# Kernel tuning notes

Measured on AMD Instinct MI355X. Metric: run time of the kernel, lower is better.

Reference implementation:

```python
import jax, jax.numpy as jnp
import numpy as np

EMB = 256
HEADS = 4
HD = EMB // HEADS
BS, SZ = 4, 64


def _layernorm(x, g, b, eps=1e-5):
    mu = jnp.mean(x, axis=-1, keepdims=True)
    var = jnp.mean((x - mu) ** 2, axis=-1, keepdims=True)
    return (x - mu) * jax.lax.rsqrt(var + eps) * g + b


def setup_inputs() -> dict:
    key = jax.random.key(0)
    ks = jax.random.split(key, 12)
    s = lambda k, shape, sc: jax.random.normal(k, shape, jnp.float32) * sc
    return {
        "x": s(ks[0], (BS, EMB, SZ, SZ), 1.0),
        "ln1_g": jnp.ones((EMB,), jnp.float32),
        "ln1_b": jnp.zeros((EMB,), jnp.float32),
        "wq": s(ks[1], (HD, HD), HD ** -0.5), "bq": jnp.zeros((HD,), jnp.float32),
        "wk": s(ks[2], (HD, HD), HD ** -0.5), "bk": jnp.zeros((HD,), jnp.float32),
        "wv": s(ks[3], (HD, HD), HD ** -0.5), "bv": jnp.zeros((HD,), jnp.float32),
        "wo": s(ks[4], (EMB, EMB), EMB ** -0.5), "bo": jnp.zeros((EMB,), jnp.float32),
        "ln2_g": jnp.ones((EMB,), jnp.float32),
        "ln2_b": jnp.zeros((EMB,), jnp.float32),
        "w1": s(ks[5], (EMB, EMB), EMB ** -0.5), "b1": jnp.zeros((EMB,), jnp.float32),
        "w2": s(ks[6], (EMB, EMB), EMB ** -0.5), "b2": jnp.zeros((EMB,), jnp.float32),
    }


def reference(x, ln1_g, ln1_b, wq, bq, wk, bk, wv, bv, wo, bo, ln2_g, ln2_b, w1, b1, w2, b2):
    bs, c, sz, _ = x.shape
    seq = sz * sz
    xt = x.reshape(bs, c, seq).swapaxes(1, 2)  # [b, s, c]
    xn = _layernorm(xt, ln1_g, ln1_b)
    # split heads: [b, h, s, d]
    h = xn.reshape(bs, seq, HEADS, HD).transpose(0, 2, 1, 3)
    q = h @ wq + bq
    k = h @ wk + bk
    v = h @ wv + bv
    scores = jnp.einsum("bhqd,bhkd->bhqk", q, k) / (HD ** 0.5)
    attn = jax.nn.softmax(scores, axis=-1)
    o = jnp.einsum("bhqk,bhkd->bhqd", attn, v)
    o = o.transpose(0, 2, 1, 3).reshape(bs, seq, c)
    o = o @ wo + bo
    av = o + xt  # residual 1
    ff = _layernorm(av, ln2_g, ln2_b) @ w1 + b1
    ff = jax.nn.gelu(ff, approximate=False) @ w2 + b2
    out = ff + av  # residual 2
    return out.swapaxes(1, 2).reshape(bs, c, sz, sz)
```

## Files before the change

### kernel.cpp

```cpp
#include <hip/hip_runtime.h>
#include <hip/hip_bf16.h>
#include <cstdint>

typedef __attribute__((ext_vector_type(8))) short short8;
typedef __attribute__((ext_vector_type(4))) short short4_;
typedef __attribute__((ext_vector_type(4))) float float4_;

#define MFMA16(a,b,c)  __builtin_amdgcn_mfma_f32_16x16x32_bf16(a,b,c,0,0,0)
#define MFMA16K16(a,b,c) __builtin_amdgcn_mfma_f32_16x16x16bf16_1k(a,b,c,0,0,0)
#define EXP2(x) __builtin_amdgcn_exp2f(x)

__device__ __forceinline__ short f2bs(float f) {
    union { float f; uint32_t u; } c;
    c.f = f;
    c.u += 0x7FFF + ((c.u >> 16) & 1);
    return (short)(c.u >> 16);
}
__device__ __forceinline__ float s2f(short s) {
    union { uint32_t u; float f; } c;
    c.u = ((uint32_t)(uint16_t)s) << 16;
    return c.f;
}

static const int EMB = 256;
static const int SEQ = 4096;
static const int TOK = 16384;

#define QSCALE 0.18033688011112042f

__global__ __launch_bounds__(256) void repack_kernel(
    const float* wq, const float* wk, const float* wv,
    const float* wo, const float* w1, const float* w2,
    short* wqT, short* wkT, short* wvT, short* woT, short* w1T, short* w2T)
{
    int idx = blockIdx.x * 256 + threadIdx.x;
    if (idx < 3 * 4096) {
        int m = idx / 4096, r = idx % 4096;
        int n = r / 64, k = r % 64;
        const float* src = (m == 0) ? wq : (m == 1) ? wk : wv;
        short* dst = (m == 0) ? wqT : (m == 1) ? wkT : wvT;
        float v = src[k * 64 + n];
        if (m == 0) v *= QSCALE;
        dst[n * 64 + k] = f2bs(v);
    } else {
        int idx2 = idx - 3 * 4096;
        if (idx2 < 3 * 65536) {
            int m = idx2 / 65536, r = idx2 % 65536;
            int n = r / 256, k = r % 256;
            const float* src = (m == 0) ? wo : (m == 1) ? w1 : w2;
            short* dst = (m == 0) ? woT : (m == 1) ? w1T : w2T;
            dst[n * 256 + k] = f2bs(src[k * 256 + n]);
        }
    }
}

__global__ __launch_bounds__(64) void ln1_kernel(
    const float* x, const float* g, const float* bta,
    short* xn, short* xt)
{
    int t = blockIdx.x * 64 + threadIdx.x;
    int b = t >> 12, sp = t & 4095;
    const float* xb = x + (size_t)b * EMB * SEQ + sp;
    float sum = 0.f, ss = 0.f;
#pragma unroll 32
    for (int c = 0; c < 256; c++) {
        float v = xb[(size_t)c * SEQ];
        sum += v; ss += v * v;
    }
    float mu = sum * (1.f / 256.f);
    float var = ss * (1.f / 256.f) - mu * mu;
    float rs = rsqrtf(var + 1e-5f);
    short* xnr = xn + (size_t)t * 256;
    short* xtr = xt + (size_t)t * 256;
#pragma unroll 8
    for (int c = 0; c < 256; c += 4) {
        short4_ ra, na;
#pragma unroll
        for (int j = 0; j < 4; j++) {
            float v = xb[(size_t)(c + j) * SEQ];
            ra[j] = f2bs(v);
            na[j] = f2bs((v - mu) * rs * g[c + j] + bta[c + j]);
        }
        *(short4_*)(xtr + c) = ra;
        *(short4_*)(xnr + c) = na;
    }
}

__global__ __launch_bounds__(256) void qkv_kernel(
    const short* xn, const short* wqT, const short* wkT, const short* wvT,
    const float* bq, const float* bk, const float* bv,
    short* qo, short* ko, short* vto)
{
    int tid = threadIdx.x;
    int w = tid >> 6, lane = tid & 63, quad = lane >> 4, l15 = lane & 15;
    int m0 = blockIdx.x * 64 + w * 16;
    int row = m0 + l15;
    int bb = row >> 12;
    int s0 = (m0 & 4095) + quad * 4;

    short8 a0[4], a1[4];
#pragma unroll
    for (int h = 0; h < 4; h++) {
        a0[h] = *(const short8*)(xn + (size_t)row * 256 + h * 64 + quad * 8);
        a1[h] = *(const short8*)(xn + (size_t)row * 256 + h * 64 + 32 + quad * 8);
    }

#pragma unroll
    for (int p = 0; p < 3; p++) {
        const short* WT = (p == 0) ? wqT : (p == 1) ? wkT : wvT;
        const float* bias = (p == 0) ? bq : (p == 1) ? bk : bv;
        float bscale = (p == 0) ? QSCALE : 1.f;
#pragma unroll
        for (int nb = 0; nb < 4; nb++) {
            int col = nb * 16 + l15;
            short8 b0 = *(const short8*)(WT + col * 64 + quad * 8);
            short8 b1 = *(const short8*)(WT + col * 64 + 32 + quad * 8);
            float bvv = bias[col] * bscale;
#pragma unroll
            for (int h = 0; h < 4; h++) {
                float4_ acc = {bvv, bvv, bvv, bvv};
                acc = MFMA16(a0[h], b0, acc);
                acc = MFMA16(a1[h], b1, acc);
                size_t headbase = (size_t)(bb * 4 + h) * SEQ;
                if (p < 2) {
                    short* dst = (p == 0) ? qo : ko;
#pragma unroll
                    for (int r = 0; r < 4; r++)
                        dst[(headbase + s0 + r) * 64 + col] = f2bs(acc[r]);
                } else {
                    short4_ pk;
#pragma unroll
                    for (int r = 0; r < 4; r++) pk[r] = f2bs(acc[r]);
                    *(short4_*)(vto + ((size_t)(bb * 4 + h) * 64 + col) * SEQ + s0) = pk;
                }
            }
        }
    }
}

__global__ __launch_bounds__(256, 4) void flash_kernel(
    const short* q, const short* k, const short* vt,
    short* O0, short* O1, float* l0, float* l1)
{
    __shared__ short K_lds[64 * 64];
    __shared__ short V_lds[64 * 64];

    int tid = threadIdx.x;
    int w = tid >> 6, lane = tid & 63, quad = lane >> 4, l15 = lane & 15;
    int qt = blockIdx.x, bh = blockIdx.y, grp = blockIdx.z;
    int span = 64 / gridDim.z;

    const short* qb = q + (size_t)bh * SEQ * 64;
    const short* kb = k + (size_t)bh * SEQ * 64 + (size_t)grp * span * 64 * 64;
    const short* vb = vt + (size_t)bh * 64 * SEQ + grp * span * 64;

    int qrow0 = qt * 128 + w * 32 + l15;
    int qrow1 = qrow0 + 16;
    short8 qA0 = *(const short8*)(qb + (size_t)qrow0 * 64 + quad * 8);
    short8 qA1 = *(const short8*)(qb + (size_t)qrow0 * 64 + 32 + quad * 8);
    short8 qB0 = *(const short8*)(qb + (size_t)qrow1 * 64 + quad * 8);
    short8 qB1 = *(const short8*)(qb + (size_t)qrow1 * 64 + 32 + quad * 8);

    float4_ oacc0[4], oacc1[4];
#pragma unroll
    for (int md = 0; md < 4; md++) {
        oacc0[md] = {0.f, 0.f, 0.f, 0.f};
        oacc1[md] = {0.f, 0.f, 0.f, 0.f};
    }
    float li0 = 0.f, li1 = 0.f;

    int srow = tid >> 2;
    int sr7 = srow & 7;
    int c0 = tid & 3;
    int l7 = l15 & 7;

    for (int kt = 0; kt < span; kt++) {
        __syncthreads();
#pragma unroll
        for (int i = 0; i < 2; i++) {
            int c = c0 + 4 * i;
            int dc = (c ^ sr7) << 3;
            *(short8*)&K_lds[srow * 64 + dc] =
                *(const short8*)(kb + (size_t)(kt * 64 + srow) * 64 + c * 8);
            *(short8*)&V_lds[srow * 64 + dc] =
                *(const short8*)(vb + (size_t)srow * SEQ + kt * 64 + c * 8);
        }
        __syncthreads();

        float4_ s0[4], s1[4];
#pragma unroll
        for (int nb = 0; nb < 4; nb++) {
            short8 k0 = *(const short8*)&K_lds[(nb * 16 + l15) * 64 + ((quad ^ l7) << 3)];
            short8 k1 = *(const short8*)&K_lds[(nb * 16 + l15) * 64 + (((quad + 4) ^ l7) << 3)];
            float4_ a = {0.f, 0.f, 0.f, 0.f};
            a = MFMA16(k0, qA0, a);
            a = MFMA16(k1, qA1, a);
            s0[nb] = a;
            float4_ b = {0.f, 0.f, 0.f, 0.f};
            b = MFMA16(k0, qB0, b);
            b = MFMA16(k1, qB1, b);
            s1[nb] = b;
        }

        short4_ pf0[4], pf1[4];
#pragma unroll
        for (int nb = 0; nb < 4; nb++)
#pragma unroll
            for (int r = 0; r < 4; r++) {
                float p0 = EXP2(s0[nb][r]);
                float p1 = EXP2(s1[nb][r]);
                li0 += p0; li1 += p1;
                pf0[nb][r] = f2bs(p0);
                pf1[nb][r] = f2bs(p1);
            }

#pragma unroll
        for (int md = 0; md < 4; md++)
#pragma unroll
            for (int nb = 0; nb < 4; nb++) {
                int c = nb * 2 + (quad >> 1);
                short4_ vf = *(const short4_*)&V_lds[(md * 16 + l15) * 64 +
                                                     ((c ^ l7) << 3) + ((quad & 1) << 2)];
                oacc0[md] = MFMA16K16(vf, pf0[nb], oacc0[md]);
                oacc1[md] = MFMA16K16(vf, pf1[nb], oacc1[md]);
            }
    }

    li0 += __shfl_xor(li0, 16);
    li0 += __shfl_xor(li0, 32);
    li1 += __shfl_xor(li1, 16);
    li1 += __shfl_xor(li1, 32);

    short* Op = grp ? O1 : O0;
    float* lp = grp ? l1 : l0;
    if (quad == 0) {
        lp[bh * 4096 + qrow0] = li0;
        lp[bh * 4096 + qrow1] = li1;
    }

    size_t ob0 = ((size_t)bh * 4096 + qrow0) * 64;
    size_t ob1 = ((size_t)bh * 4096 + qrow1) * 64;
#pragma unroll
    for (int md = 0; md < 4; md++) {
        short4_ pk0, pk1;
#pragma unroll
        for (int r = 0; r < 4; r++) {
            pk0[r] = f2bs(oacc0[md][r]);
            pk1[r] = f2bs(oacc1[md][r]);
        }
        *(short4_*)(Op + ob0 + md * 16 + quad * 4) = pk0;
        *(short4_*)(Op + ob1 + md * 16 + quad * 4) = pk1;
    }
}

__global__ __launch_bounds__(256) void combine_kernel(
    const short* O0, const short* O1, const float* l0, const float* l1,
    short* Oout, int two)
{
    int g = blockIdx.x * 256 + threadIdx.x;
    int qi = g >> 4;
    short4_ a = *(const short4_*)(O0 + (size_t)g * 4);
    float l = l0[qi];
    float4_ acc = {s2f(a[0]), s2f(a[1]), s2f(a[2]), s2f(a[3])};
    if (two) {
        short4_ b = *(const short4_*)(O1 + (size_t)g * 4);
        l += l1[qi];
#pragma unroll
        for (int j = 0; j < 4; j++) acc[j] += s2f(b[j]);
    }
    float inv = 1.f / l;
    short4_ pk;
#pragma unroll
    for (int j = 0; j < 4; j++) pk[j] = f2bs(acc[j] * inv);
    *(short4_*)(Oout + (size_t)g * 4) = pk;
}

__global__ __launch_bounds__(256) void mlp_kernel(
    const short* O,
    const short* woT, const short* w1T, const short* w2T,
    const float* bo, const float* b1, const float* b2,
    const float* g2, const float* be2,
    const short* xt, float* outf)
{
    __shared__ __align__(16) char smem[3 * 8448 + 128];
    short* av = (short*)smem;
    short* x2 = (short*)(smem + 8448);
    short* ff = (short*)(smem + 16896);
    float* stats = (float*)(smem + 25344);
    float* T = (float*)smem;

    int tid = threadIdx.x;
    int w = tid >> 6, lane = tid & 63, quad = lane >> 4, l15 = lane & 15;
    int m0 = blockIdx.x * 16;
    int n0 = w * 64;
    int arow = m0 + l15;
    int bbA = arow >> 12, spA = arow & 4095;

    float4_ acc[4];
#pragma unroll
    for (int nb = 0; nb < 4; nb++) {
        float bvv = bo[n0 + nb * 16 + l15];
        acc[nb] = {bvv, bvv, bvv, bvv};
    }
    for (int kc = 0; kc < 8; kc++) {
        int h = kc >> 1;
        int off = (kc & 1) * 32 + quad * 8;
        short8 a = *(const short8*)(O + ((size_t)(bbA * 4 + h) * 4096 + spA) * 64 + off);
#pragma unroll
        for (int nb = 0; nb < 4; nb++) {
            short8 b = *(const short8*)(woT + (size_t)(n0 + nb * 16 + l15) * 256 + kc * 32 + quad * 8);
            acc[nb] = MFMA16(a, b, acc[nb]);
        }
    }
#pragma unroll
    for (int nb = 0; nb < 4; nb++) {
        int col = n0 + nb * 16 + l15;
#pragma unroll
        for (int r = 0; r < 4; r++) {
            size_t t = (size_t)m0 + quad * 4 + r;
            av[(quad * 4 + r) * 264 + col] = f2bs(acc[nb][r] + s2f(xt[t * 256 + col]));
        }
    }
    __syncthreads();

    {
        int row = tid >> 4, sub = tid & 15;
        float sum = 0.f, ss = 0.f;
        short8 v0 = *(const short8*)&av[row * 264 + sub * 16];
        short8 v1 = *(const short8*)&av[row * 264 + sub * 16 + 8];
#pragma unroll
        for (int j = 0; j < 8; j++) {
            float a = s2f(v0[j]), b = s2f(v1[j]);
            sum += a + b; ss += a * a + b * b;
        }
#pragma unroll
        for (int off = 1; off < 16; off <<= 1) {
            sum += __shfl_xor(sum, off);
            ss += __shfl_xor(ss, off);
        }
        if (sub == 0) {
            float mu = sum * (1.f / 256.f);
            float var = ss * (1.f / 256.f) - mu * mu;
            stats[row] = mu;
            stats[16 + row] = rsqrtf(var + 1e-5f);
        }
    }
    __syncthreads();

    {
        int row = tid >> 4, sub = tid & 15;
        float mu = stats[row], rs = stats[16 + row];
#pragma unroll
        for (int j = 0; j < 16; j += 4) {
            int c = sub * 16 + j;
            short4_ rv = *(const short4_*)&av[row * 264 + c];
            short4_ pk;
#pragma unroll
            for (int i = 0; i < 4; i++)
                pk[i] = f2bs((s2f(rv[i]) - mu) * rs * g2[c + i] + be2[c + i]);
            *(short4_*)&x2[row * 264 + c] = pk;
        }
    }
    __syncthreads();

#pragma unroll
    for (int nb = 0; nb < 4; nb++) {
        float bvv = b1[n0 + nb * 16 + l15];
        acc[nb] = {bvv, bvv, bvv, bvv};
    }
    for (int kc = 0; kc < 8; kc++) {
        short8 a = *(const short8*)&x2[l15 * 264 + kc * 32 + quad * 8];
#pragma unroll
        for (int nb = 0; nb < 4; nb++) {
            short8 b = *(const short8*)(w1T + (size_t)(n0 + nb * 16 + l15) * 256 + kc * 32 + quad * 8);
            acc[nb] = MFMA16(a, b, acc[nb]);
        }
    }
#pragma unroll
    for (int nb = 0; nb < 4; nb++) {
        int col = n0 + nb * 16 + l15;
#pragma unroll
        for (int r = 0; r < 4; r++) {
            float v = acc[nb][r];
            v = 0.5f * v * (1.f + erff(v * 0.70710678118f));
            ff[(quad * 4 + r) * 264 + col] = f2bs(v);
        }
    }
    __syncthreads();

#pragma unroll
    for (int nb = 0; nb < 4; nb++) {
        float bvv = b2[n0 + nb * 16 + l15];
        acc[nb] = {bvv, bvv, bvv, bvv};
    }
    for (int kc = 0; kc < 8; kc++) {
        short8 a = *(const short8*)&ff[l15 * 264 + kc * 32 + quad * 8];
#pragma unroll
        for (int nb = 0; nb < 4; nb++) {
            short8 b = *(const short8*)(w2T + (size_t)(n0 + nb * 16 + l15) * 256 + kc * 32 + quad * 8);
            acc[nb] = MFMA16(a, b, acc[nb]);
        }
    }
    float vout[4][4];
#pragma unroll
    for (int nb = 0; nb < 4; nb++) {
        int col = n0 + nb * 16 + l15;
#pragma unroll
        for (int r = 0; r < 4; r++)
            vout[nb][r] = acc[nb][r] + s2f(av[(quad * 4 + r) * 264 + col]);
    }
    __syncthreads();

    float* tw = T + w * 1040;
#pragma unroll
    for (int nb = 0; nb < 4; nb++)
#pragma unroll
        for (int r = 0; r < 4; r++)
            tw[(quad * 4 + r) * 65 + nb * 16 + l15] = vout[nb][r];

    int bb = m0 >> 12;
    int spb = m0 & 4095;
    float* dst = outf + ((size_t)bb * 256 + n0 + lane) * SEQ + spb;
#pragma unroll
    for (int j = 0; j < 16; j += 4) {
        float4_ pk = {tw[(j + 0) * 65 + lane], tw[(j + 1) * 65 + lane],
                      tw[(j + 2) * 65 + lane], tw[(j + 3) * 65 + lane]};
        *(float4_*)(dst + j) = pk;
    }
}

extern "C" void kernel_launch(void* const* d_in, const int* in_sizes, int n_in,
                              void* d_out, int out_size, void* d_ws, size_t ws_size,
                              hipStream_t stream)
{
    const float* x     = (const float*)d_in[0];
    const float* ln1_g = (const float*)d_in[1];
    const float* ln1_b = (const float*)d_in[2];
    const float* wq    = (const float*)d_in[3];
    const float* bq    = (const float*)d_in[4];
    const float* wk    = (const float*)d_in[5];
    const float* bk    = (const float*)d_in[6];
    const float* wv    = (const float*)d_in[7];
    const float* bv    = (const float*)d_in[8];
    const float* wo    = (const float*)d_in[9];
    const float* bo    = (const float*)d_in[10];
    const float* ln2_g = (const float*)d_in[11];
    const float* ln2_b = (const float*)d_in[12];
    const float* w1    = (const float*)d_in[13];
    const float* b1    = (const float*)d_in[14];
    const float* w2    = (const float*)d_in[15];
    const float* b2    = (const float*)d_in[16];

    char* ws = (char*)d_ws;
    const size_t SZ_BF = (size_t)TOK * 256 * 2;

    short* wqT = (short*)(ws + 0);
    short* wkT = (short*)(ws + 8192);
    short* wvT = (short*)(ws + 16384);
    short* woT = (short*)(ws + 24576);
    short* w1T = (short*)(ws + 155648);
    short* w2T = (short*)(ws + 286720);
    char* base = ws + 524288;

    short* xt  = (short*)(base);
    short* kbuf= (short*)(base + SZ_BF);
    short* vtb = (short*)(base + 2 * SZ_BF);
    float* l0  = (float*)(base + 3 * SZ_BF);
    float* l1  = (float*)(base + 3 * SZ_BF + 262144);
    short* O1  = (short*)(base + 3 * SZ_BF + 524288);

    const size_t NEED_SPLIT = 524288 + 3 * SZ_BF + 524288 + SZ_BF;
    int nz = (ws_size >= NEED_SPLIT) ? 2 : 1;

    short* qb  = (short*)d_out;
    short* xn  = (short*)((char*)d_out + SZ_BF);
    short* O0  = xn;
    short* Onrm= vtb;

    repack_kernel<<<816, 256, 0, stream>>>(wq, wk, wv, wo, w1, w2,
                                           wqT, wkT, wvT, woT, w1T, w2T);
    ln1_kernel<<<TOK / 64, 64, 0, stream>>>(x, ln1_g, ln1_b, xn, xt);
    qkv_kernel<<<TOK / 64, 256, 0, stream>>>(xn, wqT, wkT, wvT, bq, bk, bv,
                                             qb, kbuf, vtb);
    flash_kernel<<<dim3(32, 16, nz), 256, 0, stream>>>(qb, kbuf, vtb, O0, O1, l0, l1);
    combine_kernel<<<4096, 256, 0, stream>>>(O0, O1, l0, l1, Onrm, nz - 1);
    mlp_kernel<<<TOK / 16, 256, 0, stream>>>(Onrm, woT, w1T, w2T, bo, b1, b2,
                                             ln2_g, ln2_b, xt, (float*)d_out);
}
```

Before: 290.0 us.

## Prefetch next K/V tile into registers and use packed bf16 conversion

The global loads for the next K/V tile are issued into registers before the current tile's compute, which overlaps global memory latency with the MFMA work. One of the two barriers is replaced by an explicit LDS waitcnt plus s_barrier. Separately, the manual round-to-nearest float-to-bf16 conversion of the softmax probabilities is replaced with the hardware v_cvt_pk_bf16_f32 instruction, and the row-sum accumulation is reassociated into a tree. The prefetch raises register pressure, and the barrier change relies on the hand-written waitcnt being correct.

New measurement: 288.9 us. Within noise of the previous version (-0.4%).

```diff
diff --git a/kernel.cpp b/kernel.cpp
--- a/kernel.cpp
+++ b/kernel.cpp
@@ -174,18 +174,29 @@
     int c0 = tid & 3;
     int l7 = l15 & 7;
 
+    int dcA = (c0 ^ sr7) << 3;
+    int dcB = ((c0 + 4) ^ sr7) << 3;
+
+    short8 kr0 = *(const short8*)(kb + (size_t)srow * 64 + c0 * 8);
+    short8 kr1 = *(const short8*)(kb + (size_t)srow * 64 + (c0 + 4) * 8);
+    short8 vr0 = *(const short8*)(vb + (size_t)srow * SEQ + c0 * 8);
+    short8 vr1 = *(const short8*)(vb + (size_t)srow * SEQ + (c0 + 4) * 8);
+
     for (int kt = 0; kt < span; kt++) {
         __syncthreads();
-#pragma unroll
-        for (int i = 0; i < 2; i++) {
-            int c = c0 + 4 * i;
-            int dc = (c ^ sr7) << 3;
-            *(short8*)&K_lds[srow * 64 + dc] =
-                *(const short8*)(kb + (size_t)(kt * 64 + srow) * 64 + c * 8);
-            *(short8*)&V_lds[srow * 64 + dc] =
-                *(const short8*)(vb + (size_t)srow * SEQ + kt * 64 + c * 8);
-        }
-        __syncthreads();
+        *(short8*)&K_lds[srow * 64 + dcA] = kr0;
+        *(short8*)&K_lds[srow * 64 + dcB] = kr1;
+        *(short8*)&V_lds[srow * 64 + dcA] = vr0;
+        *(short8*)&V_lds[srow * 64 + dcB] = vr1;
+        if (kt + 1 < span) {
+            kr0 = *(const short8*)(kb + (size_t)((kt + 1) * 64 + srow) * 64 + c0 * 8);
+            kr1 = *(const short8*)(kb + (size_t)((kt + 1) * 64 + srow) * 64 + (c0 + 4) * 8);
+            vr0 = *(const short8*)(vb + (size_t)srow * SEQ + (kt + 1) * 64 + c0 * 8);
+            vr1 = *(const short8*)(vb + (size_t)srow * SEQ + (kt + 1) * 64 + (c0 + 4) * 8);
+        }
+        asm volatile("s_waitcnt lgkmcnt(0)" ::: "memory");
+        __builtin_amdgcn_s_barrier();
+        asm volatile("" ::: "memory");
 
         float4_ s0[4], s1[4];
 #pragma unroll
@@ -204,15 +215,21 @@
 
         short4_ pf0[4], pf1[4];
 #pragma unroll
-        for (int nb = 0; nb < 4; nb++)
-#pragma unroll
-            for (int r = 0; r < 4; r++) {
-                float p0 = EXP2(s0[nb][r]);
-                float p1 = EXP2(s1[nb][r]);
-                li0 += p0; li1 += p1;
-                pf0[nb][r] = f2bs(p0);
-                pf1[nb][r] = f2bs(p1);
-            }
+        for (int nb = 0; nb < 4; nb++) {
+            float p00 = EXP2(s0[nb][0]), p01 = EXP2(s0[nb][1]);
+            float p02 = EXP2(s0[nb][2]), p03 = EXP2(s0[nb][3]);
+            li0 += (p00 + p01) + (p02 + p03);
+            float p10 = EXP2(s1[nb][0]), p11 = EXP2(s1[nb][1]);
+            float p12 = EXP2(s1[nb][2]), p13 = EXP2(s1[nb][3]);
+            li1 += (p10 + p11) + (p12 + p13);
+            union { short4_ s; uint32_t u[2]; } pa, pb;
+            asm("v_cvt_pk_bf16_f32 %0, %1, %2" : "=v"(pa.u[0]) : "v"(p00), "v"(p01));
+            asm("v_cvt_pk_bf16_f32 %0, %1, %2" : "=v"(pa.u[1]) : "v"(p02), "v"(p03));
+            asm("v_cvt_pk_bf16_f32 %0, %1, %2" : "=v"(pb.u[0]) : "v"(p10), "v"(p11));
+            asm("v_cvt_pk_bf16_f32 %0, %1, %2" : "=v"(pb.u[1]) : "v"(p12), "v"(p13));
+            pf0[nb] = pa.s;
+            pf1[nb] = pb.s;
+        }
 
 #pragma unroll
         for (int md = 0; md < 4; md++)
```
